# Optimization experiments

Hardware: AMD Instinct MI355X
Metric: run time of the kernel (lower is better)

## Reference

```python
import jax, jax.numpy as jnp
import numpy as np

SIZE = 64          # node feature dim
T = 12             # num edge styles
N = 4000           # notes (nodes)
B = 1              # graph batch (torch branch requires B==1)
S2 = SIZE          # secondary_size == size (secondary_size=0 default)


def setup_inputs() -> dict:
    key = jax.random.key(0)
    ks = jax.random.split(key, 5)
    std_a = (2.0 / (S2 + S2)) ** 0.5
    std_b = (2.0 / (SIZE + S2)) ** 0.5
    std_c = (2.0 / (SIZE * T + S2)) ** 0.5
    x = jax.random.normal(ks[0], (B, N, SIZE), jnp.float32)
    # dense per-edge-type adjacency; scaled so repeated propagation stays bounded
    edge_matrix = jax.random.normal(ks[1], (T, N, N), jnp.float32) / np.float32(np.sqrt(N))
    ba = jnp.zeros((T, SIZE), jnp.float32)
    bw = jnp.zeros((3 * S2,), jnp.float32)
    wz_wr_wh = std_c * jax.random.normal(ks[2], (T, SIZE, 3 * S2), jnp.float32)
    uz_ur = std_b * jax.random.normal(ks[3], (SIZE, 2 * S2), jnp.float32)
    uh = std_a * jax.random.normal(ks[4], (S2, S2), jnp.float32)
    return dict(x=x, edge_matrix=edge_matrix, ba=ba, bw=bw,
                wz_wr_wh=wz_wr_wh, uz_ur=uz_ur, uh=uh, iteration=10)


def reference(x, edge_matrix, ba, bw, wz_wr_wh, uz_ur, uh, iteration):
    h = x  # [B, N, S]
    for _ in range(iteration):
        # per-edge-type propagation: edge_matrix[t].T @ h  -> [B, T, N, S]
        act = jnp.einsum('tnm,bns->btms', edge_matrix, h) + ba[None, :, None, :]
        # fused z/r/h projection per edge type: [B, T, N, 3*S2]
        awzrh = jnp.einsum('btms,tsk->btmk', act, wz_wr_wh) + bw
        awz, awr, awh = jnp.split(awzrh, 3, axis=-1)
        awz = awz.sum(1)  # sum over edge types -> [B, N, S2]
        awr = awr.sum(1)
        awh = awh.sum(1)
        uzr = h @ uz_ur                      # [B, N, 2*S2]
        uz, ur = jnp.split(uzr, 2, axis=-1)
        z = jax.nn.sigmoid(awz + uz)
        r = jax.nn.sigmoid(awr + ur)
        hh = jnp.tanh(awh + (r * h) @ uh)    # secondary_size == size branch
        h = (1.0 - z) * h + z * hh
    return h
```

## Files before the change

### kernel.cpp

```cpp
#include <hip/hip_runtime.h>
#include <stdint.h>

#define NN 4000
#define SD 64
#define TT 12
#define NITER 10
#define KP 4032
#define NKB 63
#define NMT 63

typedef _Float16 f16;
typedef _Float16 f16x8 __attribute__((ext_vector_type(8)));
typedef float    f32x4 __attribute__((ext_vector_type(4)));

__global__ void wconv_kernel(const float* __restrict__ w, f16* __restrict__ wt) {
    int idx = blockIdx.x * 256 + threadIdx.x;
    if (idx >= TT * SD * 192) return;
    int t = idx / (SD * 192);
    int rem = idx - t * SD * 192;
    int s = rem / 192;
    int j = rem - s * 192;
    wt[t * 192 * SD + j * SD + s] = (f16)w[idx];
}

__global__ void init_kernel(const float* __restrict__ x, float* __restrict__ h32,
                            f16* __restrict__ hT) {
    int idx = blockIdx.x * 256 + threadIdx.x;
    if (idx < NN * SD) {
        float v = x[idx];
        h32[idx] = v;
        int n = idx >> 6, s = idx & 63;
        hT[(size_t)s * KP + n] = (f16)v;
    } else {
        int r = idx - NN * SD;
        if (r < SD * 32) {
            int s = r >> 5, k = NN + (r & 31);
            hT[(size_t)s * KP + k] = (f16)0.f;
        }
    }
}

__global__ __launch_bounds__(256) void econv_kernel(const float* __restrict__ E,
                                                    f16* __restrict__ Ec) {
    __shared__ f16 lsT[64][72];
    const int mt = blockIdx.x, kb = blockIdx.y, t = blockIdx.z;
    const int tid = threadIdx.x;
    const int kr0 = tid >> 4;
    const int mc  = (tid & 15) << 2;
    const int gmb = mt * 64 + mc;
    #pragma unroll
    for (int p = 0; p < 4; ++p) {
        int kr = kr0 + p * 16;
        int k  = kb * 64 + kr;
        float4 v = {0.f, 0.f, 0.f, 0.f};
        if (k < NN) {
            const float* src = E + ((size_t)t * NN + k) * NN + gmb;
            if (gmb + 3 < NN) v = *(const float4*)src;
            else {
                if (gmb + 0 < NN) v.x = src[0];
                if (gmb + 1 < NN) v.y = src[1];
                if (gmb + 2 < NN) v.z = src[2];
                if (gmb + 3 < NN) v.w = src[3];
            }
        }
        lsT[mc + 0][kr] = (f16)v.x;
        lsT[mc + 1][kr] = (f16)v.y;
        lsT[mc + 2][kr] = (f16)v.z;
        lsT[mc + 3][kr] = (f16)v.w;
    }
    __syncthreads();
    f16* dstb = Ec + ((size_t)(t * NKB + kb) * KP + mt * 64) * 64;
    #pragma unroll
    for (int p = 0; p < 2; ++p) {
        int m  = (tid >> 3) + p * 32;
        int kc = tid & 7;
        uint4 w = *(const uint4*)&lsT[m][kc * 8];
        *(uint4*)(dstb + m * 64 + kc * 8) = w;
    }
}

__global__ __launch_bounds__(256) void gemm_kernel(
        const f16*  __restrict__ Ec,
        const f16*  __restrict__ hT,
        const float* __restrict__ ba,
        const f16*  __restrict__ Wt,
        float*      __restrict__ slab)
{
    __shared__ char arena[36864];
    f16*      lsA   = (f16*)(arena);
    f16*      lsB   = (f16*)(arena + 9216);
    f16*      lsAct = (f16*)(arena);
    uint32_t* lsW   = (uint32_t*)(arena + 9216);

    const int t    = blockIdx.y;
    const int mi   = blockIdx.x;
    const int tid  = threadIdx.x;
    const int wave = tid >> 6;
    const int lane = tid & 63;
    const int l15  = lane & 15;
    const int quad = lane >> 4;
    const int am   = tid >> 3;
    const int akc  = tid & 7;

    f32x4 acc[4];
    #pragma unroll
    for (int si = 0; si < 4; ++si) { f32x4 z = {0.f,0.f,0.f,0.f}; acc[si] = z; }

    const f16* Bthr = hT + (size_t)am * KP + akc * 8;

    for (int kb = 0; kb < NKB; ++kb) {
        const f16* Asrc = Ec + ((size_t)(t * NKB + kb) * KP + mi * 64) * 64 + tid * 8;
        const uint4 a0 = *(const uint4*)(Asrc);
        const uint4 a1 = *(const uint4*)(Asrc + 2048);
        const f16* Bsrc = Bthr + kb * 64;
        const uint4 b0 = *(const uint4*)(Bsrc);
        const uint4 b1 = *(const uint4*)(Bsrc + (size_t)32 * KP);
        *(uint4*)&lsA[(am +  0) * 72 + akc * 8] = a0;
        *(uint4*)&lsA[(am + 32) * 72 + akc * 8] = a1;
        *(uint4*)&lsB[(am +  0) * 72 + akc * 8] = b0;
        *(uint4*)&lsB[(am + 32) * 72 + akc * 8] = b1;
        __syncthreads();
        #pragma unroll
        for (int k2 = 0; k2 < 64; k2 += 32) {
            const f16x8 af = *(const f16x8*)&lsA[(wave * 16 + l15) * 72 + k2 + quad * 8];
            #pragma unroll
            for (int si = 0; si < 4; ++si) {
                const f16x8 bf = *(const f16x8*)&lsB[(si * 16 + l15) * 72 + k2 + quad * 8];
                acc[si] = __builtin_amdgcn_mfma_f32_16x16x32_f16(af, bf, acc[si], 0, 0, 0);
            }
        }
        __syncthreads();
    }

    const int mrow = wave * 16 + quad * 4;
    #pragma unroll
    for (int si = 0; si < 4; ++si) {
        const float bav = ba[t * SD + si * 16 + l15];
        #pragma unroll
        for (int r = 0; r < 4; ++r)
            lsAct[(mrow + r) * 72 + si * 16 + l15] = (f16)(acc[si][r] + bav);
    }
    {
        const uint32_t* wsrc = (const uint32_t*)(Wt + (size_t)t * 192 * SD);
        #pragma unroll
        for (int i = 0; i < 6; ++i) {
            int c  = tid + 256 * i;
            int j  = c >> 3;
            int ch = c & 7;
            *(uint4*)&lsW[j * 36 + ch * 4] = *(const uint4*)(wsrc + j * 32 + ch * 4);
        }
    }
    __syncthreads();

    f32x4 acc2[12];
    #pragma unroll
    for (int jf = 0; jf < 12; ++jf) { f32x4 z = {0.f,0.f,0.f,0.f}; acc2[jf] = z; }
    #pragma unroll
    for (int k2 = 0; k2 < 64; k2 += 32) {
        const f16x8 a2 = *(const f16x8*)&lsAct[(wave * 16 + l15) * 72 + k2 + quad * 8];
        #pragma unroll
        for (int jf = 0; jf < 12; ++jf) {
            const f16x8 b2 = *(const f16x8*)&lsW[(jf * 16 + l15) * 36 + (k2 >> 1) + quad * 4];
            acc2[jf] = __builtin_amdgcn_mfma_f32_16x16x32_f16(a2, b2, acc2[jf], 0, 0, 0);
        }
    }
    float* sb = slab + (size_t)t * NN * 192;
    #pragma unroll
    for (int jf = 0; jf < 12; ++jf) {
        #pragma unroll
        for (int r = 0; r < 4; ++r) {
            const int m = mi * 64 + mrow + r;
            if (m < NN)
                sb[(size_t)m * 192 + jf * 16 + l15] = acc2[jf][r];
        }
    }
}

__global__ __launch_bounds__(256) void gru_kernel(
        const float* __restrict__ slab, const float* __restrict__ bw,
        const float* __restrict__ uzur, const float* __restrict__ uhm,
        const float* __restrict__ hin, float* __restrict__ hout,
        f16* __restrict__ hT) {
    __shared__ float uz_s[64][128];
    __shared__ float uh_s[64][65];
    __shared__ float h_s[32][65];
    __shared__ float uzr_s[32][130];
    __shared__ float rh_s[32][65];

    const int tid = threadIdx.x;
    const int n0  = blockIdx.x * 32;

    #pragma unroll
    for (int i = 0; i < 8; ++i) {
        int idx4 = tid + 256 * i;
        int k = idx4 >> 5;
        int c = (idx4 & 31) << 2;
        *(float4*)&uz_s[k][c] = *(const float4*)(uzur + (idx4 << 2));
    }
    #pragma unroll
    for (int i = 0; i < 4; ++i) {
        int idx4 = tid + 256 * i;
        int k = idx4 >> 4;
        int s = (idx4 & 15) << 2;
        float4 v = *(const float4*)(uhm + (idx4 << 2));
        uh_s[k][s] = v.x; uh_s[k][s+1] = v.y; uh_s[k][s+2] = v.z; uh_s[k][s+3] = v.w;
    }
    #pragma unroll
    for (int i = 0; i < 8; ++i) {
        int e = tid + 256 * i;
        int n = e >> 6, s = e & 63;
        h_s[n][s] = hin[(size_t)(n0 + n) * SD + s];
    }
    __syncthreads();

    {
        const int nd = tid & 31;
        const int c0 = (tid >> 5) << 4;
        float a[16];
        #pragma unroll
        for (int i = 0; i < 16; ++i) a[i] = 0.f;
        for (int k = 0; k < 64; ++k) {
            const float hv = h_s[nd][k];
            #pragma unroll
            for (int i = 0; i < 16; ++i) a[i] += hv * uz_s[k][c0 + i];
        }
        #pragma unroll
        for (int i = 0; i < 16; ++i) uzr_s[nd][c0 + i] = a[i];
    }
    __syncthreads();

    const int node = tid >> 3;
    const int sc   = (tid & 7) << 3;
    const int gn   = n0 + node;

    float az[8], ar[8], ah[8];
    #pragma unroll
    for (int i = 0; i < 8; ++i) { az[i] = 0.f; ar[i] = 0.f; ah[i] = 0.f; }
    for (int t = 0; t < TT; ++t) {
        const float* ab = slab + (size_t)t * NN * 192 + (size_t)gn * 192;
        float4 v;
        v = *(const float4*)(ab + sc);        az[0]+=v.x; az[1]+=v.y; az[2]+=v.z; az[3]+=v.w;
        v = *(const float4*)(ab + sc + 4);    az[4]+=v.x; az[5]+=v.y; az[6]+=v.z; az[7]+=v.w;
        v = *(const float4*)(ab + 64 + sc);   ar[0]+=v.x; ar[1]+=v.y; ar[2]+=v.z; ar[3]+=v.w;
        v = *(const float4*)(ab + 64 + sc+4); ar[4]+=v.x; ar[5]+=v.y; ar[6]+=v.z; ar[7]+=v.w;
        v = *(const float4*)(ab + 128 + sc);  ah[0]+=v.x; ah[1]+=v.y; ah[2]+=v.z; ah[3]+=v.w;
        v = *(const float4*)(ab + 128 + sc+4);ah[4]+=v.x; ah[5]+=v.y; ah[6]+=v.z; ah[7]+=v.w;
    }

    float z[8], r[8];
    #pragma unroll
    for (int i = 0; i < 8; ++i) {
        const float azv = az[i] + 12.f * bw[sc + i];
        const float arv = ar[i] + 12.f * bw[64 + sc + i];
        z[i] = 1.f / (1.f + __expf(-(azv + uzr_s[node][sc + i])));
        r[i] = 1.f / (1.f + __expf(-(arv + uzr_s[node][64 + sc + i])));
        rh_s[node][sc + i] = r[i] * h_s[node][sc + i];
    }
    __syncthreads();
    float a2[8];
    #pragma unroll
    for (int i = 0; i < 8; ++i) a2[i] = 0.f;
    for (int k = 0; k < 64; ++k) {
        const float rv = rh_s[node][k];
        #pragma unroll
        for (int i = 0; i < 8; ++i) a2[i] += rv * uh_s[k][sc + i];
    }
    #pragma unroll
    for (int i = 0; i < 8; ++i) {
        const float ahv = ah[i] + 12.f * bw[128 + sc + i];
        const float hh = tanhf(ahv + a2[i]);
        const float hv = h_s[node][sc + i];
        const float hn = (1.f - z[i]) * hv + z[i] * hh;
        hout[(size_t)gn * SD + sc + i] = hn;
        hT[(size_t)(sc + i) * KP + gn] = (f16)hn;
    }
}

extern "C" void kernel_launch(void* const* d_in, const int* in_sizes, int n_in,
                              void* d_out, int out_size, void* d_ws, size_t ws_size,
                              hipStream_t stream) {
    const float* x    = (const float*)d_in[0];
    const float* E    = (const float*)d_in[1];
    const float* ba   = (const float*)d_in[2];
    const float* bw   = (const float*)d_in[3];
    const float* W    = (const float*)d_in[4];
    const float* uzur = (const float*)d_in[5];
    const float* uhm  = (const float*)d_in[6];
    float* out = (float*)d_out;

    char* ws = (char*)d_ws;
    float* h32  = (float*)(ws);
    f16*   hT   = (f16*)(ws + (1 << 20));
    f16*   Wt   = (f16*)(ws + (1 << 20) + (1 << 19));
    float* slab = (float*)(ws + (2 << 20));
    f16*   Ec   = (f16*)(ws + (size_t)41943040);

    wconv_kernel<<<dim3(576), dim3(256), 0, stream>>>(W, Wt);
    init_kernel<<<dim3(1009), dim3(256), 0, stream>>>(x, h32, hT);
    econv_kernel<<<dim3(NMT, NKB, TT), dim3(256), 0, stream>>>(E, Ec);
    for (int it = 0; it < NITER; ++it) {
        gemm_kernel<<<dim3(NMT, TT), dim3(256), 0, stream>>>(Ec, hT, ba, Wt, slab);
        float* ho = (it == NITER - 1) ? out : h32;
        gru_kernel<<<dim3(125), dim3(256), 0, stream>>>(slab, bw, uzur, uhm, h32, ho, hT);
    }
}
```

Before: 2.254 ms.

## Double-buffer GEMM tiles via direct global-to-LDS loads with XOR-swizzled layouts

The main GEMM loop now stages the A and B tiles with global_load_lds DMA into two LDS buffers, so the next k-block is fetched while MFMAs run on the current one. To make this work, Ec, the hidden-state transpose and the weight layout are all re-stored in a blocked, XOR-swizzled format that is written by econv, init, gru and wconv. Padding is replaced by swizzling to avoid LDS bank conflicts. This adds manual waitcnt and barrier handling, whose correctness depends on the hand-encoded counter values.

```diff
diff --git a/kernel.cpp b/kernel.cpp
--- a/kernel.cpp
+++ b/kernel.cpp
@@ -13,6 +13,12 @@
 typedef _Float16 f16x8 __attribute__((ext_vector_type(8)));
 typedef float    f32x4 __attribute__((ext_vector_type(4)));
 
+__device__ __forceinline__ void dma16(const void* g, void* l) {
+    __builtin_amdgcn_global_load_lds(
+        (const __attribute__((address_space(1))) uint32_t*)g,
+        (__attribute__((address_space(3))) uint32_t*)l, 16, 0, 0);
+}
+
 __global__ void wconv_kernel(const float* __restrict__ w, f16* __restrict__ wt) {
     int idx = blockIdx.x * 256 + threadIdx.x;
     if (idx >= TT * SD * 192) return;
@@ -20,23 +26,22 @@
     int rem = idx - t * SD * 192;
     int s = rem / 192;
     int j = rem - s * 192;
-    wt[t * 192 * SD + j * SD + s] = (f16)w[idx];
+    wt[t * 192 * 64 + j * 64 + (((s >> 3) ^ (j & 7)) << 3) + (s & 7)] = (f16)w[idx];
 }
 
 __global__ void init_kernel(const float* __restrict__ x, float* __restrict__ h32,
-                            f16* __restrict__ hT) {
+                            f16* __restrict__ hTb) {
     int idx = blockIdx.x * 256 + threadIdx.x;
-    if (idx < NN * SD) {
-        float v = x[idx];
-        h32[idx] = v;
-        int n = idx >> 6, s = idx & 63;
-        hT[(size_t)s * KP + n] = (f16)v;
-    } else {
-        int r = idx - NN * SD;
-        if (r < SD * 32) {
-            int s = r >> 5, k = NN + (r & 31);
-            hT[(size_t)s * KP + k] = (f16)0.f;
-        }
+    if (idx < NN * SD) h32[idx] = x[idx];
+    if (idx < NKB * 64 * 64) {
+        int row = idx >> 6;
+        int s   = row & 63;
+        int kb  = row >> 6;
+        int p   = idx & 63;
+        int pc  = p >> 3, pos = p & 7;
+        int kk  = ((pc ^ (s & 7)) << 3) + pos;
+        int n   = kb * 64 + kk;
+        hTb[idx] = (n < NN) ? (f16)x[n * SD + s] : (f16)0.f;
     }
 }
 
@@ -75,79 +80,92 @@
         int m  = (tid >> 3) + p * 32;
         int kc = tid & 7;
         uint4 w = *(const uint4*)&lsT[m][kc * 8];
-        *(uint4*)(dstb + m * 64 + kc * 8) = w;
-    }
-}
-
-__global__ __launch_bounds__(256) void gemm_kernel(
+        *(uint4*)(dstb + m * 64 + ((kc ^ (m & 7)) << 3)) = w;
+    }
+}
+
+__global__ __launch_bounds__(256, 4) void gemm_kernel(
         const f16*  __restrict__ Ec,
-        const f16*  __restrict__ hT,
+        const f16*  __restrict__ hTb,
         const float* __restrict__ ba,
         const f16*  __restrict__ Wt,
         float*      __restrict__ slab)
 {
-    __shared__ char arena[36864];
-    f16*      lsA   = (f16*)(arena);
-    f16*      lsB   = (f16*)(arena + 9216);
-    f16*      lsAct = (f16*)(arena);
-    uint32_t* lsW   = (uint32_t*)(arena + 9216);
+    __shared__ __align__(16) char arena[32768];
 
     const int t    = blockIdx.y;
     const int mi   = blockIdx.x;
     const int tid  = threadIdx.x;
-    const int wave = tid >> 6;
+    const int w    = tid >> 6;
     const int lane = tid & 63;
     const int l15  = lane & 15;
     const int quad = lane >> 4;
-    const int am   = tid >> 3;
-    const int akc  = tid & 7;
+    const int rA   = w * 16 + l15;
+    const int swz  = l15 & 7;
+
+    const char*  Ag    = (const char*)(Ec + ((size_t)t * NKB * KP + (size_t)mi * 64) * 64);
+    const char*  Bg    = (const char*)hTb;
+    const size_t Astep = (size_t)KP * 64 * sizeof(f16);
+    const int    wo    = w * 2048 + lane * 16;
+    const int    wl    = w * 2048;
+
+    dma16(Ag + wo,        arena + wl);
+    dma16(Ag + wo + 1024, arena + wl + 1024);
+    dma16(Bg + wo,        arena + 16384 + wl);
+    dma16(Bg + wo + 1024, arena + 16384 + wl + 1024);
 
     f32x4 acc[4];
     #pragma unroll
     for (int si = 0; si < 4; ++si) { f32x4 z = {0.f,0.f,0.f,0.f}; acc[si] = z; }
 
-    const f16* Bthr = hT + (size_t)am * KP + akc * 8;
-
     for (int kb = 0; kb < NKB; ++kb) {
-        const f16* Asrc = Ec + ((size_t)(t * NKB + kb) * KP + mi * 64) * 64 + tid * 8;
-        const uint4 a0 = *(const uint4*)(Asrc);
-        const uint4 a1 = *(const uint4*)(Asrc + 2048);
-        const f16* Bsrc = Bthr + kb * 64;
-        const uint4 b0 = *(const uint4*)(Bsrc);
-        const uint4 b1 = *(const uint4*)(Bsrc + (size_t)32 * KP);
-        *(uint4*)&lsA[(am +  0) * 72 + akc * 8] = a0;
-        *(uint4*)&lsA[(am + 32) * 72 + akc * 8] = a1;
-        *(uint4*)&lsB[(am +  0) * 72 + akc * 8] = b0;
-        *(uint4*)&lsB[(am + 32) * 72 + akc * 8] = b1;
-        __syncthreads();
-        #pragma unroll
-        for (int k2 = 0; k2 < 64; k2 += 32) {
-            const f16x8 af = *(const f16x8*)&lsA[(wave * 16 + l15) * 72 + k2 + quad * 8];
+        const int cur = kb & 1;
+        if (kb + 1 < NKB) {
+            const char* a = Ag + (size_t)(kb + 1) * Astep;
+            const char* b = Bg + (size_t)(kb + 1) * 8192;
+            const int nb  = (cur ^ 1) * 8192;
+            dma16(a + wo,        arena + nb + wl);
+            dma16(a + wo + 1024, arena + nb + wl + 1024);
+            dma16(b + wo,        arena + 16384 + nb + wl);
+            dma16(b + wo + 1024, arena + 16384 + nb + wl + 1024);
+            __builtin_amdgcn_s_waitcnt(0x0F74);
+        } else {
+            __builtin_amdgcn_s_waitcnt(0x0F70);
+        }
+        __builtin_amdgcn_s_barrier();
+        const f16* Ab = (const f16*)(arena + cur * 8192);
+        const f16* Bb = (const f16*)(arena + 16384 + cur * 8192);
+        #pragma unroll
+        for (int kh = 0; kh < 2; ++kh) {
+            const int cA = quad + kh * 4;
+            const f16x8 af = *(const f16x8*)(Ab + rA * 64 + ((cA ^ swz) << 3));
             #pragma unroll
             for (int si = 0; si < 4; ++si) {
-                const f16x8 bf = *(const f16x8*)&lsB[(si * 16 + l15) * 72 + k2 + quad * 8];
+                const int rB = si * 16 + l15;
+                const f16x8 bf = *(const f16x8*)(Bb + rB * 64 + ((cA ^ swz) << 3));
                 acc[si] = __builtin_amdgcn_mfma_f32_16x16x32_f16(af, bf, acc[si], 0, 0, 0);
             }
         }
-        __syncthreads();
-    }
-
-    const int mrow = wave * 16 + quad * 4;
+        __builtin_amdgcn_s_barrier();
+    }
+
+    {
+        const char* Wg = (const char*)(Wt + (size_t)t * 192 * 64);
+        #pragma unroll
+        for (int i = 0; i < 6; ++i)
+            dma16(Wg + w * 6144 + i * 1024 + lane * 16, arena + 8192 + w * 6144 + i * 1024);
+    }
+    const int mrow = w * 16 + quad * 4;
+    f16* actb = (f16*)arena;
     #pragma unroll
     for (int si = 0; si < 4; ++si) {
         const float bav = ba[t * SD + si * 16 + l15];
-        #pragma unroll
-        for (int r = 0; r < 4; ++r)
-            lsAct[(mrow + r) * 72 + si * 16 + l15] = (f16)(acc[si][r] + bav);
-    }
-    {
-        const uint32_t* wsrc = (const uint32_t*)(Wt + (size_t)t * 192 * SD);
-        #pragma unroll
-        for (int i = 0; i < 6; ++i) {
-            int c  = tid + 256 * i;
-            int j  = c >> 3;
-            int ch = c & 7;
-            *(uint4*)&lsW[j * 36 + ch * 4] = *(const uint4*)(wsrc + j * 32 + ch * 4);
+        const int col = si * 16 + l15;
+        const int cc  = col >> 3, pos = col & 7;
+        #pragma unroll
+        for (int r = 0; r < 4; ++r) {
+            const int m = mrow + r;
+            actb[m * 64 + (((cc ^ (m & 7)) << 3)) + pos] = (f16)(acc[si][r] + bav);
         }
     }
     __syncthreads();
@@ -155,12 +173,15 @@
     f32x4 acc2[12];
     #pragma unroll
     for (int jf = 0; jf < 12; ++jf) { f32x4 z = {0.f,0.f,0.f,0.f}; acc2[jf] = z; }
-    #pragma unroll
-    for (int k2 = 0; k2 < 64; k2 += 32) {
-        const f16x8 a2 = *(const f16x8*)&lsAct[(wave * 16 + l15) * 72 + k2 + quad * 8];
+    const f16* Wl = (const f16*)(arena + 8192);
+    #pragma unroll
+    for (int kh = 0; kh < 2; ++kh) {
+        const int c2 = quad + kh * 4;
+        const f16x8 a2 = *(const f16x8*)(actb + rA * 64 + ((c2 ^ swz) << 3));
         #pragma unroll
         for (int jf = 0; jf < 12; ++jf) {
-            const f16x8 b2 = *(const f16x8*)&lsW[(jf * 16 + l15) * 36 + (k2 >> 1) + quad * 4];
+            const int j = jf * 16 + l15;
+            const f16x8 b2 = *(const f16x8*)(Wl + j * 64 + ((c2 ^ swz) << 3));
             acc2[jf] = __builtin_amdgcn_mfma_f32_16x16x32_f16(a2, b2, acc2[jf], 0, 0, 0);
         }
     }
@@ -180,7 +201,7 @@
         const float* __restrict__ slab, const float* __restrict__ bw,
         const float* __restrict__ uzur, const float* __restrict__ uhm,
         const float* __restrict__ hin, float* __restrict__ hout,
-        f16* __restrict__ hT) {
+        f16* __restrict__ hTb) {
     __shared__ float uz_s[64][128];
     __shared__ float uh_s[64][65];
     __shared__ float h_s[32][65];
@@ -265,14 +286,17 @@
         #pragma unroll
         for (int i = 0; i < 8; ++i) a2[i] += rv * uh_s[k][sc + i];
     }
+    const int kb = gn >> 6, kk = gn & 63;
+    const int cc = kk >> 3, pos = kk & 7;
     #pragma unroll
     for (int i = 0; i < 8; ++i) {
         const float ahv = ah[i] + 12.f * bw[128 + sc + i];
         const float hh = tanhf(ahv + a2[i]);
         const float hv = h_s[node][sc + i];
         const float hn = (1.f - z[i]) * hv + z[i] * hh;
-        hout[(size_t)gn * SD + sc + i] = hn;
-        hT[(size_t)(sc + i) * KP + gn] = (f16)hn;
+        const int s = sc + i;
+        hout[(size_t)gn * SD + s] = hn;
+        hTb[(size_t)(kb * 64 + s) * 64 + ((cc ^ (s & 7)) << 3) + pos] = (f16)hn;
     }
 }
 
@@ -290,17 +314,17 @@
 
     char* ws = (char*)d_ws;
     float* h32  = (float*)(ws);
-    f16*   hT   = (f16*)(ws + (1 << 20));
+    f16*   hTb  = (f16*)(ws + (1 << 20));
     f16*   Wt   = (f16*)(ws + (1 << 20) + (1 << 19));
     float* slab = (float*)(ws + (2 << 20));
     f16*   Ec   = (f16*)(ws + (size_t)41943040);
 
     wconv_kernel<<<dim3(576), dim3(256), 0, stream>>>(W, Wt);
-    init_kernel<<<dim3(1009), dim3(256), 0, stream>>>(x, h32, hT);
+    init_kernel<<<dim3(1008), dim3(256), 0, stream>>>(x, h32, hTb);
     econv_kernel<<<dim3(NMT, NKB, TT), dim3(256), 0, stream>>>(E, Ec);
     for (int it = 0; it < NITER; ++it) {
-        gemm_kernel<<<dim3(NMT, TT), dim3(256), 0, stream>>>(Ec, hT, ba, Wt, slab);
+        gemm_kernel<<<dim3(NMT, TT), dim3(256), 0, stream>>>(Ec, hTb, ba, Wt, slab);
         float* ho = (it == NITER - 1) ? out : h32;
-        gru_kernel<<<dim3(125), dim3(256), 0, stream>>>(slab, bw, uzur, uhm, h32, ho, hT);
-    }
-}
+        gru_kernel<<<dim3(125), dim3(256), 0, stream>>>(slab, bw, uzur, uhm, h32, ho, hTb);
+    }
+}
```

Result: faster. 2.172 ms (-3.6%).
